# Performance work log

Hardware: AMD Instinct MI355X
Metric: run time of the kernel (lower is better)

Reference implementation:

```python
import jax, jax.numpy as jnp
import numpy as np

HIDDEN_DIM = 512  # H; hidden/encoder feature dim is 2H = 1024


def setup_inputs() -> dict:
    key = jax.random.key(0)
    k1, k2, k3, k4, k5 = jax.random.split(key, 5)
    B, S, D2, H = 16, 4096, 2 * HIDDEN_DIM, HIDDEN_DIM
    hidden = jax.random.normal(k1, (B, D2), dtype=jnp.float32)
    encoder_outputs = jax.random.normal(k2, (B, S, D2), dtype=jnp.float32)
    # nn.Linear(4H, H): weight [H, 4H] in torch; store transposed [4H, H] for x @ W
    W_attn = jax.random.normal(k3, (2 * D2, H), dtype=jnp.float32) * (1.0 / np.sqrt(2 * D2))
    b_attn = jax.random.normal(k4, (H,), dtype=jnp.float32) * 0.01
    # nn.Linear(H, 1, bias=False): weight [1, H] -> vector [H]
    w_v = jax.random.normal(k5, (H,), dtype=jnp.float32) * (1.0 / np.sqrt(H))
    return {"hidden": hidden, "encoder_outputs": encoder_outputs,
            "W_attn": W_attn, "b_attn": b_attn, "w_v": w_v}


def reference(hidden, encoder_outputs, W_attn, b_attn, w_v):
    B, S, D2 = encoder_outputs.shape
    # Broadcast decoder hidden over seq positions and concat with encoder outputs.
    hid = jnp.broadcast_to(hidden[:, None, :], (B, S, D2))
    cat = jnp.concatenate([hid, encoder_outputs], axis=2)        # [B, S, 4H]
    energy = jnp.tanh(cat @ W_attn + b_attn)                      # [B, S, H]
    scores = jnp.einsum('bsh,h->bs', energy, w_v)                 # [B, S]
    attention = jax.nn.softmax(scores, axis=1)                    # [B, S]
    context = jnp.einsum('bs,bsd->bd', attention, encoder_outputs)  # [B, 2H]
    return context
```

## Files before the change

### kernel.cpp

```cpp
#include <hip/hip_runtime.h>
#include <hip/hip_bf16.h>
#include <math.h>

#define HD   512
#define D2   1024
#define SEQ  4096
#define BAT  16
#define BM   64
#define BN   256
#define BK   32

typedef _Float16 half8 __attribute__((ext_vector_type(8)));
typedef float    f32x4 __attribute__((ext_vector_type(4)));
typedef __attribute__((address_space(3))) void lds_void_t;
typedef __attribute__((address_space(1))) void glb_void_t;

__global__ void wconv_kernel(const float* __restrict__ W, _Float16* __restrict__ WtS) {
  __shared__ float tile[32][17];
  const int kt  = blockIdx.x;
  const int nbg = blockIdx.y;
  const int nh  = nbg >> 4, nbl = nbg & 15;
  const int t   = threadIdx.x;
  {
    const int n16 = t & 15, kk = t >> 4;
    #pragma unroll
    for (int i = 0; i < 2; ++i) {
      const int k = kk + i * 16;
      tile[k][n16] = W[(size_t)(D2 + kt * 32 + k) * HD + nh * 256 + nbl * 16 + n16];
    }
  }
  __syncthreads();
  if (t < 64) {
    const int kc = t >> 4, nlo = t & 15;
    half8 h;
    #pragma unroll
    for (int j = 0; j < 8; ++j) h[j] = (_Float16)tile[kc * 8 + j][nlo];
    *(half8*)(WtS + ((size_t)(kt * 2 + nh) * 1024 + nbl * 64 + kc * 16 + nlo) * 8) = h;
  }
}

__global__ void hproj_kernel(const float* __restrict__ hidden,
                             const float* __restrict__ W,
                             float* __restrict__ hproj) {
  const int b  = blockIdx.x >> 3;
  const int kc = blockIdx.x & 7;
  const int h  = threadIdx.x;
  float a0 = 0.f, a1 = 0.f;
  #pragma unroll 4
  for (int i = 0; i < 128; ++i) {
    const int d = kc * 128 + i;
    const float hd = hidden[b * D2 + d];
    a0 += hd * W[(size_t)d * HD + h];
    a1 += hd * W[(size_t)d * HD + h + 256];
  }
  atomicAdd(&hproj[b * HD + h], a0);
  atomicAdd(&hproj[b * HD + h + 256], a1);
}

__global__ __launch_bounds__(256, 4) void scores_kernel(
    const float* __restrict__ enc, const _Float16* __restrict__ WtS,
    const float* __restrict__ hproj, const float* __restrict__ b_attn,
    const float* __restrict__ w_v, float* __restrict__ scores)
{
  __shared__ __align__(16) _Float16 As[2][BM * BK];
  __shared__ __align__(16) _Float16 Bs[2][BN * BK];

  const int s0  = blockIdx.x * BM;
  const int nh  = blockIdx.y;
  const int b   = blockIdx.z;
  const int tid = threadIdx.x, lane = tid & 63, w = tid >> 6;
  const int col = lane & 15, quad = lane >> 4;
  const int strip = w >> 1, nq2 = w & 1;

  const float* encB = enc + ((size_t)b * SEQ + s0) * D2;
  const _Float16* WtB = WtS + (size_t)nh * 1024 * 8;

  const int arow = tid >> 2, akc = tid & 3;
  const float* aSrcBase = encB + (size_t)arow * D2 + akc * 8;
  const int aDstOff = (akc * 64 + (arow ^ (akc << 2))) * 8;
  const int a0off = (quad * 64 + ((strip * 32 + col)      ^ (quad << 2))) * 8;
  const int a1off = (quad * 64 + ((strip * 32 + 16 + col) ^ (quad << 2))) * 8;

  f32x4 acc0[8], acc1[8];
  const f32x4 z = {0.f, 0.f, 0.f, 0.f};
  #pragma unroll
  for (int i = 0; i < 8; ++i) { acc0[i] = z; acc1[i] = z; }

  f32x4 Ra0, Ra1, Rb0, Rb1;

  auto loadA = [&](int kt, f32x4& v0, f32x4& v1) {
    const float* p = aSrcBase + kt * BK;
    v0 = *(const f32x4*)p;
    v1 = *(const f32x4*)(p + 4);
  };
  auto storeA = [&](int buf, const f32x4& v0, const f32x4& v1) {
    half8 h;
    h[0] = (_Float16)v0[0]; h[1] = (_Float16)v0[1];
    h[2] = (_Float16)v0[2]; h[3] = (_Float16)v0[3];
    h[4] = (_Float16)v1[0]; h[5] = (_Float16)v1[1];
    h[6] = (_Float16)v1[2]; h[7] = (_Float16)v1[3];
    *(half8*)&As[buf][aDstOff] = h;
  };
  auto issueB = [&](int kt, int buf) {
    #pragma unroll
    for (int i = 0; i < 4; ++i) {
      const int c = i * 256 + tid;
      __builtin_amdgcn_global_load_lds(
          (glb_void_t*)(WtB + (size_t)kt * 16384 + c * 8),
          (lds_void_t*)((char*)&Bs[buf][0] + c * 16), 16, 0, 0);
    }
  };
  auto compute = [&](int buf) {
    half8 a0 = *(const half8*)&As[buf][a0off];
    half8 a1 = *(const half8*)&As[buf][a1off];
    #pragma unroll
    for (int nt = 0; nt < 8; ++nt) {
      const int nbl_local = nq2 * 8 + nt;
      half8 bf = *(const half8*)&Bs[buf][(nbl_local * 64 + quad * 16 + col) * 8];
      acc0[nt] = __builtin_amdgcn_mfma_f32_16x16x32_f16(a0, bf, acc0[nt], 0, 0, 0);
      acc1[nt] = __builtin_amdgcn_mfma_f32_16x16x32_f16(a1, bf, acc1[nt], 0, 0, 0);
    }
  };

  loadA(0, Ra0, Ra1);
  storeA(0, Ra0, Ra1);
  issueB(0, 0);
  loadA(1, Rb0, Rb1);
  __syncthreads();

  #pragma unroll 2
  for (int kt = 0; kt < 32; ++kt) {
    const int cur = kt & 1, nxt = cur ^ 1;
    if (kt + 1 < 32) issueB(kt + 1, nxt);
    if (kt + 2 < 32) {
      if (kt & 1) loadA(kt + 2, Rb0, Rb1);
      else        loadA(kt + 2, Ra0, Ra1);
    }
    compute(cur);
    if (kt + 1 < 32) {
      if (kt & 1) storeA(nxt, Ra0, Ra1);
      else        storeA(nxt, Rb0, Rb1);
    }
    __syncthreads();
  }

  float p0[4] = {0.f, 0.f, 0.f, 0.f}, p1[4] = {0.f, 0.f, 0.f, 0.f};
  const float* hp = hproj + b * HD + nh * 256;
  #pragma unroll
  for (int nt = 0; nt < 8; ++nt) {
    const int nl = nq2 * 128 + nt * 16 + col;
    const float hb = hp[nl] + b_attn[nh * 256 + nl];
    const float wv = w_v[nh * 256 + nl];
    #pragma unroll
    for (int r = 0; r < 4; ++r) {
      {
        float x = fminf(fmaxf(acc0[nt][r] + hb, -15.f), 15.f);
        float ex = __expf(2.f * x);
        p0[r] += wv * __fdividef(ex - 1.f, ex + 1.f);
      }
      {
        float x = fminf(fmaxf(acc1[nt][r] + hb, -15.f), 15.f);
        float ex = __expf(2.f * x);
        p1[r] += wv * __fdividef(ex - 1.f, ex + 1.f);
      }
    }
  }
  #pragma unroll
  for (int off = 8; off >= 1; off >>= 1) {
    #pragma unroll
    for (int r = 0; r < 4; ++r) {
      p0[r] += __shfl_xor(p0[r], off, 64);
      p1[r] += __shfl_xor(p1[r], off, 64);
    }
  }
  if (col == 0) {
    const int m0 = s0 + strip * 32 + quad * 4;
    #pragma unroll
    for (int r = 0; r < 4; ++r) {
      atomicAdd(&scores[b * SEQ + m0 + r], p0[r]);
      atomicAdd(&scores[b * SEQ + m0 + 16 + r], p1[r]);
    }
  }
}

__global__ void softmax_kernel(float* __restrict__ scores) {
  const int b = blockIdx.x;
  float* sc = scores + b * SEQ;
  __shared__ float red[16];
  const int tid = threadIdx.x;
  float loc[16];
  float mx = -1e30f;
  #pragma unroll
  for (int i = 0; i < 16; ++i) { loc[i] = sc[i * 256 + tid]; mx = fmaxf(mx, loc[i]); }
  #pragma unroll
  for (int off = 32; off >= 1; off >>= 1) mx = fmaxf(mx, __shfl_xor(mx, off, 64));
  if ((tid & 63) == 0) red[tid >> 6] = mx;
  __syncthreads();
  mx = fmaxf(fmaxf(red[0], red[1]), fmaxf(red[2], red[3]));
  float sum = 0.f;
  #pragma unroll
  for (int i = 0; i < 16; ++i) { loc[i] = __expf(loc[i] - mx); sum += loc[i]; }
  #pragma unroll
  for (int off = 32; off >= 1; off >>= 1) sum += __shfl_xor(sum, off, 64);
  if ((tid & 63) == 0) red[8 + (tid >> 6)] = sum;
  __syncthreads();
  sum = red[8] + red[9] + red[10] + red[11];
  const float inv = 1.0f / sum;
  #pragma unroll
  for (int i = 0; i < 16; ++i) sc[i * 256 + tid] = loc[i] * inv;
}

__global__ __launch_bounds__(256) void context_kernel(const float* __restrict__ attn,
                                                      const float* __restrict__ enc,
                                                      float* __restrict__ out) {
  const int b  = blockIdx.y;
  const int s0 = blockIdx.x * 64;
  const int tid = threadIdx.x;
  const float* encB = enc + ((size_t)b * SEQ + s0) * D2 + tid * 4;
  const float* at   = attn + b * SEQ + s0;
  f32x4 acc0 = {0.f, 0.f, 0.f, 0.f}, acc1 = {0.f, 0.f, 0.f, 0.f};
  #pragma unroll 8
  for (int i = 0; i < 64; i += 2) {
    acc0 += at[i]     * *(const f32x4*)(encB + (size_t)i * D2);
    acc1 += at[i + 1] * *(const f32x4*)(encB + (size_t)(i + 1) * D2);
  }
  f32x4 acc = acc0 + acc1;
  float* o = out + b * D2 + tid * 4;
  atomicAdd(o + 0, acc[0]);
  atomicAdd(o + 1, acc[1]);
  atomicAdd(o + 2, acc[2]);
  atomicAdd(o + 3, acc[3]);
}

extern "C" void kernel_launch(void* const* d_in, const int* in_sizes, int n_in,
                              void* d_out, int out_size, void* d_ws, size_t ws_size,
                              hipStream_t stream) {
  (void)in_sizes; (void)n_in; (void)ws_size;
  const float* hidden = (const float*)d_in[0];
  const float* enc    = (const float*)d_in[1];
  const float* W      = (const float*)d_in[2];
  const float* b_attn = (const float*)d_in[3];
  const float* w_v    = (const float*)d_in[4];
  float* out = (float*)d_out;

  char* ws = (char*)d_ws;
  _Float16* WtS = (_Float16*)ws;
  float* hproj  = (float*)(ws + (1 << 20));
  float* scores = (float*)(ws + (1 << 20) + 32768);

  hipMemsetAsync(d_out, 0, (size_t)out_size * sizeof(float), stream);
  hipMemsetAsync(hproj, 0, BAT * HD * sizeof(float), stream);
  hipMemsetAsync(scores, 0, (size_t)BAT * SEQ * sizeof(float), stream);

  wconv_kernel  <<<dim3(32, 32),            256, 0, stream>>>(W, WtS);
  hproj_kernel  <<<dim3(128),               256, 0, stream>>>(hidden, W, hproj);
  scores_kernel <<<dim3(SEQ / BM, 2, BAT),  256, 0, stream>>>(enc, WtS, hproj, b_attn, w_v, scores);
  softmax_kernel<<<dim3(BAT),               256, 0, stream>>>(scores);
  context_kernel<<<dim3(SEQ / 64, BAT),     256, 0, stream>>>(scores, enc, out);
}
```

Measured before the change: 491.1 us.

## Widen scores GEMM tile to full N with 3-stage async LDS pipeline

The scores kernel now covers all 512 hidden columns per block with 128-row M tiles and 512 threads. Before, the N dimension was split across two blocks, so each block read the fp32 encoder tile twice. The encoder tile is now copied straight to LDS as fp32 through global_load_lds, using an XOR swizzle, and converted to fp16 at fragment-load time. A triple-buffered pipeline with explicit vmcnt waits replaces the old register staging and double buffer. The costs are more LDS per block (fp32 A tile, three stages) and higher register pressure from 32 accumulators per thread, which may lower occupancy.

```diff
diff --git a/kernel.cpp b/kernel.cpp
--- a/kernel.cpp
+++ b/kernel.cpp
@@ -6,9 +6,9 @@
 #define D2   1024
 #define SEQ  4096
 #define BAT  16
-#define BM   64
-#define BN   256
+#define BM   128
 #define BK   32
+#define NKT  32
 
 typedef _Float16 half8 __attribute__((ext_vector_type(8)));
 typedef float    f32x4 __attribute__((ext_vector_type(4)));
@@ -57,129 +57,127 @@
   atomicAdd(&hproj[b * HD + h + 256], a1);
 }
 
-__global__ __launch_bounds__(256, 4) void scores_kernel(
+__global__ __launch_bounds__(512, 2) void scores_kernel(
     const float* __restrict__ enc, const _Float16* __restrict__ WtS,
     const float* __restrict__ hproj, const float* __restrict__ b_attn,
     const float* __restrict__ w_v, float* __restrict__ scores)
 {
-  __shared__ __align__(16) _Float16 As[2][BM * BK];
-  __shared__ __align__(16) _Float16 Bs[2][BN * BK];
+  __shared__ __align__(16) float    As[3][BM * BK];
+  __shared__ __align__(16) _Float16 Bs[3][2048 * 8];
 
   const int s0  = blockIdx.x * BM;
-  const int nh  = blockIdx.y;
-  const int b   = blockIdx.z;
+  const int b   = blockIdx.y;
   const int tid = threadIdx.x, lane = tid & 63, w = tid >> 6;
-  const int col = lane & 15, quad = lane >> 4;
-  const int strip = w >> 1, nq2 = w & 1;
+  const int col16 = lane & 15, q = lane >> 4;
+  const int wm = w >> 2, wn = w & 3;
 
   const float* encB = enc + ((size_t)b * SEQ + s0) * D2;
-  const _Float16* WtB = WtS + (size_t)nh * 1024 * 8;
-
-  const int arow = tid >> 2, akc = tid & 3;
-  const float* aSrcBase = encB + (size_t)arow * D2 + akc * 8;
-  const int aDstOff = (akc * 64 + (arow ^ (akc << 2))) * 8;
-  const int a0off = (quad * 64 + ((strip * 32 + col)      ^ (quad << 2))) * 8;
-  const int a1off = (quad * 64 + ((strip * 32 + 16 + col) ^ (quad << 2))) * 8;
-
-  f32x4 acc0[8], acc1[8];
+
+  f32x4 acc[4][8];
   const f32x4 z = {0.f, 0.f, 0.f, 0.f};
   #pragma unroll
-  for (int i = 0; i < 8; ++i) { acc0[i] = z; acc1[i] = z; }
-
-  f32x4 Ra0, Ra1, Rb0, Rb1;
-
-  auto loadA = [&](int kt, f32x4& v0, f32x4& v1) {
-    const float* p = aSrcBase + kt * BK;
-    v0 = *(const f32x4*)p;
-    v1 = *(const f32x4*)(p + 4);
+  for (int mi = 0; mi < 4; ++mi)
+    #pragma unroll
+    for (int ni = 0; ni < 8; ++ni) acc[mi][ni] = z;
+
+  auto stage = [&](int kt, int buf) {
+    const float* ek = encB + kt * BK;
+    #pragma unroll
+    for (int i = 0; i < 2; ++i) {
+      const int s = i * 512 + tid;
+      const int row = s >> 3;
+      const int g = (s & 7) ^ (row & 7);
+      __builtin_amdgcn_global_load_lds((glb_void_t*)(ek + (size_t)row * D2 + g * 4),
+          (lds_void_t*)((char*)&As[buf][0] + s * 16), 16, 0, 0);
+    }
+    const _Float16* wk = WtS + (size_t)kt * 16384;
+    #pragma unroll
+    for (int i = 0; i < 4; ++i) {
+      const int c = i * 512 + tid;
+      __builtin_amdgcn_global_load_lds((glb_void_t*)(wk + c * 8),
+          (lds_void_t*)((char*)&Bs[buf][0] + c * 16), 16, 0, 0);
+    }
   };
-  auto storeA = [&](int buf, const f32x4& v0, const f32x4& v1) {
-    half8 h;
-    h[0] = (_Float16)v0[0]; h[1] = (_Float16)v0[1];
-    h[2] = (_Float16)v0[2]; h[3] = (_Float16)v0[3];
-    h[4] = (_Float16)v1[0]; h[5] = (_Float16)v1[1];
-    h[6] = (_Float16)v1[2]; h[7] = (_Float16)v1[3];
-    *(half8*)&As[buf][aDstOff] = h;
+
+  auto compute = [&](int buf) {
+    const float* pA = &As[buf][0];
+    const _Float16* pB = &Bs[buf][0];
+    half8 af[4];
+    #pragma unroll
+    for (int mi = 0; mi < 4; ++mi) {
+      const int row = wm * 64 + mi * 16 + col16;
+      const int rb = row * 8, rx = row & 7;
+      const f32x4 lo = *(const f32x4*)&pA[(rb + ((2 * q)     ^ rx)) * 4];
+      const f32x4 hi = *(const f32x4*)&pA[(rb + ((2 * q + 1) ^ rx)) * 4];
+      half8 h;
+      h[0] = (_Float16)lo[0]; h[1] = (_Float16)lo[1];
+      h[2] = (_Float16)lo[2]; h[3] = (_Float16)lo[3];
+      h[4] = (_Float16)hi[0]; h[5] = (_Float16)hi[1];
+      h[6] = (_Float16)hi[2]; h[7] = (_Float16)hi[3];
+      af[mi] = h;
+    }
+    #pragma unroll
+    for (int ni = 0; ni < 8; ++ni) {
+      const half8 bf = *(const half8*)&pB[((wn * 8 + ni) * 64 + q * 16 + col16) * 8];
+      #pragma unroll
+      for (int mi = 0; mi < 4; ++mi)
+        acc[mi][ni] = __builtin_amdgcn_mfma_f32_16x16x32_f16(af[mi], bf, acc[mi][ni], 0, 0, 0);
+    }
   };
-  auto issueB = [&](int kt, int buf) {
-    #pragma unroll
-    for (int i = 0; i < 4; ++i) {
-      const int c = i * 256 + tid;
-      __builtin_amdgcn_global_load_lds(
-          (glb_void_t*)(WtB + (size_t)kt * 16384 + c * 8),
-          (lds_void_t*)((char*)&Bs[buf][0] + c * 16), 16, 0, 0);
-    }
-  };
-  auto compute = [&](int buf) {
-    half8 a0 = *(const half8*)&As[buf][a0off];
-    half8 a1 = *(const half8*)&As[buf][a1off];
-    #pragma unroll
-    for (int nt = 0; nt < 8; ++nt) {
-      const int nbl_local = nq2 * 8 + nt;
-      half8 bf = *(const half8*)&Bs[buf][(nbl_local * 64 + quad * 16 + col) * 8];
-      acc0[nt] = __builtin_amdgcn_mfma_f32_16x16x32_f16(a0, bf, acc0[nt], 0, 0, 0);
-      acc1[nt] = __builtin_amdgcn_mfma_f32_16x16x32_f16(a1, bf, acc1[nt], 0, 0, 0);
-    }
-  };
-
-  loadA(0, Ra0, Ra1);
-  storeA(0, Ra0, Ra1);
-  issueB(0, 0);
-  loadA(1, Rb0, Rb1);
-  __syncthreads();
-
-  #pragma unroll 2
-  for (int kt = 0; kt < 32; ++kt) {
-    const int cur = kt & 1, nxt = cur ^ 1;
-    if (kt + 1 < 32) issueB(kt + 1, nxt);
-    if (kt + 2 < 32) {
-      if (kt & 1) loadA(kt + 2, Rb0, Rb1);
-      else        loadA(kt + 2, Ra0, Ra1);
-    }
-    compute(cur);
-    if (kt + 1 < 32) {
-      if (kt & 1) storeA(nxt, Ra0, Ra1);
-      else        storeA(nxt, Rb0, Rb1);
-    }
-    __syncthreads();
-  }
-
-  float p0[4] = {0.f, 0.f, 0.f, 0.f}, p1[4] = {0.f, 0.f, 0.f, 0.f};
-  const float* hp = hproj + b * HD + nh * 256;
-  #pragma unroll
-  for (int nt = 0; nt < 8; ++nt) {
-    const int nl = nq2 * 128 + nt * 16 + col;
-    const float hb = hp[nl] + b_attn[nh * 256 + nl];
-    const float wv = w_v[nh * 256 + nl];
-    #pragma unroll
-    for (int r = 0; r < 4; ++r) {
-      {
-        float x = fminf(fmaxf(acc0[nt][r] + hb, -15.f), 15.f);
+
+  stage(0, 0);
+  stage(1, 1);
+  asm volatile("s_waitcnt vmcnt(6)" ::: "memory");
+  __builtin_amdgcn_s_barrier();
+
+  #pragma unroll 3
+  for (int kt = 0; kt < NKT - 2; ++kt) {
+    stage(kt + 2, (kt + 2) % 3);
+    compute(kt % 3);
+    asm volatile("s_waitcnt vmcnt(6)" ::: "memory");
+    __builtin_amdgcn_s_barrier();
+  }
+  compute((NKT - 2) % 3);
+  asm volatile("s_waitcnt vmcnt(0)" ::: "memory");
+  __builtin_amdgcn_s_barrier();
+  compute((NKT - 1) % 3);
+
+  float p[4][4];
+  #pragma unroll
+  for (int mi = 0; mi < 4; ++mi)
+    #pragma unroll
+    for (int r = 0; r < 4; ++r) p[mi][r] = 0.f;
+
+  #pragma unroll
+  for (int ni = 0; ni < 8; ++ni) {
+    const int n = wn * 128 + ni * 16 + col16;
+    const float hb = hproj[b * HD + n] + b_attn[n];
+    const float wv = w_v[n];
+    #pragma unroll
+    for (int mi = 0; mi < 4; ++mi) {
+      #pragma unroll
+      for (int r = 0; r < 4; ++r) {
+        float x = fminf(fmaxf(acc[mi][ni][r] + hb, -15.f), 15.f);
         float ex = __expf(2.f * x);
-        p0[r] += wv * __fdividef(ex - 1.f, ex + 1.f);
+        p[mi][r] += wv * __fdividef(ex - 1.f, ex + 1.f);
       }
-      {
-        float x = fminf(fmaxf(acc1[nt][r] + hb, -15.f), 15.f);
-        float ex = __expf(2.f * x);
-        p1[r] += wv * __fdividef(ex - 1.f, ex + 1.f);
-      }
     }
   }
   #pragma unroll
   for (int off = 8; off >= 1; off >>= 1) {
     #pragma unroll
-    for (int r = 0; r < 4; ++r) {
-      p0[r] += __shfl_xor(p0[r], off, 64);
-      p1[r] += __shfl_xor(p1[r], off, 64);
-    }
-  }
-  if (col == 0) {
-    const int m0 = s0 + strip * 32 + quad * 4;
-    #pragma unroll
-    for (int r = 0; r < 4; ++r) {
-      atomicAdd(&scores[b * SEQ + m0 + r], p0[r]);
-      atomicAdd(&scores[b * SEQ + m0 + 16 + r], p1[r]);
-    }
+    for (int mi = 0; mi < 4; ++mi)
+      #pragma unroll
+      for (int r = 0; r < 4; ++r)
+        p[mi][r] += __shfl_xor(p[mi][r], off, 64);
+  }
+  if (col16 == 0) {
+    const int m0 = s0 + wm * 64 + q * 4;
+    #pragma unroll
+    for (int mi = 0; mi < 4; ++mi)
+      #pragma unroll
+      for (int r = 0; r < 4; ++r)
+        atomicAdd(&scores[b * SEQ + m0 + mi * 16 + r], p[mi][r]);
   }
 }
 
@@ -252,9 +250,9 @@
   hipMemsetAsync(hproj, 0, BAT * HD * sizeof(float), stream);
   hipMemsetAsync(scores, 0, (size_t)BAT * SEQ * sizeof(float), stream);
 
-  wconv_kernel  <<<dim3(32, 32),            256, 0, stream>>>(W, WtS);
-  hproj_kernel  <<<dim3(128),               256, 0, stream>>>(hidden, W, hproj);
-  scores_kernel <<<dim3(SEQ / BM, 2, BAT),  256, 0, stream>>>(enc, WtS, hproj, b_attn, w_v, scores);
-  softmax_kernel<<<dim3(BAT),               256, 0, stream>>>(scores);
-  context_kernel<<<dim3(SEQ / 64, BAT),     256, 0, stream>>>(scores, enc, out);
-}
+  wconv_kernel  <<<dim3(32, 32),          256, 0, stream>>>(W, WtS);
+  hproj_kernel  <<<dim3(128),             256, 0, stream>>>(hidden, W, hproj);
+  scores_kernel <<<dim3(SEQ / BM, BAT),   512, 0, stream>>>(enc, WtS, hproj, b_attn, w_v, scores);
+  softmax_kernel<<<dim3(BAT),             256, 0, stream>>>(scores);
+  context_kernel<<<dim3(SEQ / 64, BAT),   256, 0, stream>>>(scores, enc, out);
+}
```

Result: no change. 486.1 us (-1.0%).
